# Optimization experiments

Measured on AMD Instinct MI355X. Metric: run time of the kernel, lower is better.

## Reference

```python
import jax, jax.numpy as jnp
import numpy as np


def setup_inputs() -> dict:
    key = jax.random.key(0)
    k1, k2 = jax.random.split(key)
    n, d, ic, oc, r = 128, 256, 16, 16, 10
    x = jax.random.normal(k1, (n, d, ic, r), dtype=jnp.float32)
    weights = jax.random.normal(k2, (d, ic, oc, r), dtype=jnp.float32)
    return {"x": x, "weights": weights}


def reference(x, weights):
    # x: [n, d, ic, r]; weights: [d, ic, oc, r]
    # log_softmax over in_channels (dim=1 of weights)
    log_weights = jax.nn.log_softmax(weights, axis=1)  # [d, ic, oc, r]
    # broadcast add: x[n,d,ic,1,r] + lw[d,ic,oc,r] -> [n,d,ic,oc,r]
    z = x[:, :, :, None, :] + log_weights[None]
    # logsumexp over ic -> [n, d, oc, r]
    return jax.nn.logsumexp(z, axis=2)
```

## Files before the change

kernel.cpp:

```cpp
#include <hip/hip_runtime.h>
#include <hip/hip_bf16.h>


typedef __attribute__((ext_vector_type(8))) short bf16x8;
typedef __attribute__((ext_vector_type(4))) float f32x4;

__device__ __forceinline__ unsigned short f2bf(float v) {
    unsigned u = __float_as_uint(v);
    u += 0x7FFF + ((u >> 16) & 1);
    return (unsigned short)(u >> 16);
}

__global__ __launch_bounds__(512, 2) void fused_mfma_kernel(const float* __restrict__ x,
                                                            const float* __restrict__ w,
                                                            float* __restrict__ out) {
    __shared__ __align__(16) unsigned short es[128 * 328];
    __shared__ __align__(16) unsigned short ws_[10 * 640];
    __shared__ float lcs[160];

    const int tid = threadIdx.x;
    const int d   = blockIdx.x;

    {
        const int n_l = tid >> 2;
        const int seg = tid & 3;
        const float* xg = x + (n_l * 256 + d) * 160 + seg * 40;
        float4 xv[10];
#pragma unroll
        for (int k = 0; k < 10; ++k) xv[k] = *reinterpret_cast<const float4*>(xg + 4 * k);
        const float* wgp = w + d * 2560 + tid * 5;
        float wv[5];
#pragma unroll
        for (int k = 0; k < 5; ++k) wv[k] = wgp[k];

        const float* xf = reinterpret_cast<const float*>(xv);
#pragma unroll
        for (int k = 0; k < 40; ++k) {
            const int icr = seg * 40 + k;
            const int ic  = icr / 10;
            const int r   = icr - ic * 10;
            es[n_l * 328 + r * 32 + ic] = f2bf(__expf(xf[k]));
        }
#pragma unroll
        for (int k = 0; k < 5; ++k) {
            const int off = tid * 5 + k;
            const int ic  = off / 160;
            const int rem = off - ic * 160;
            const int oc  = rem / 10;
            const int r   = rem - oc * 10;
            ws_[r * 640 + oc * 40 + ic] = f2bf(__expf(wv[k]));
        }
        const uint4 z = make_uint4(0u, 0u, 0u, 0u);
        for (int c = tid; c < 1280; c += 512) {
            const int n = c / 10, r = c - (c / 10) * 10;
            uint4* p = reinterpret_cast<uint4*>(&es[n * 328 + r * 32 + 16]);
            p[0] = z; p[1] = z;
        }
        if (tid < 160) {
            const int r = tid >> 4, oc = tid & 15;
            uint4* p = reinterpret_cast<uint4*>(&ws_[r * 640 + oc * 40 + 16]);
            p[0] = z; p[1] = z;
        }
    }
    __syncthreads();

    if (tid < 160) {
        const int oc = tid / 10, r = tid - (tid / 10) * 10;
        const unsigned short* p = &ws_[r * 640 + oc * 40];
        float s = 0.f;
#pragma unroll
        for (int ic = 0; ic < 16; ++ic)
            s += __uint_as_float(((unsigned)p[ic]) << 16);
        lcs[oc * 10 + r] = __logf(s);
    }

    const int mt = tid >> 6;
    const int l  = tid & 63;
    const int lm = l & 15;
    const int kg = l >> 4;

    const int abase = (mt * 16 + lm) * 328 + kg * 8;
    const int bbase = lm * 40 + kg * 8;

    f32x4 acc[10];
    const f32x4 zero = {0.f, 0.f, 0.f, 0.f};
#pragma unroll
    for (int r = 0; r < 10; ++r) {
        bf16x8 a = *reinterpret_cast<const bf16x8*>(&es[abase + r * 32]);
        bf16x8 b = *reinterpret_cast<const bf16x8*>(&ws_[r * 640 + bbase]);
        acc[r] = __builtin_amdgcn_mfma_f32_16x16x32_bf16(a, b, zero, 0, 0, 0);
    }
    __syncthreads();

    float lc[10];
#pragma unroll
    for (int r = 0; r < 10; ++r) lc[r] = lcs[lm * 10 + r];

#pragma unroll
    for (int j = 0; j < 4; ++j) {
        const int n = mt * 16 + kg * 4 + j;
        float* og = out + (n * 256 + d) * 160 + lm * 10;
#pragma unroll
        for (int h = 0; h < 5; ++h) {
            float2 o;
            o.x = __logf(acc[2 * h][j])     - lc[2 * h];
            o.y = __logf(acc[2 * h + 1][j]) - lc[2 * h + 1];
            *reinterpret_cast<float2*>(og + 2 * h) = o;
        }
    }
}

extern "C" void kernel_launch(void* const* d_in, const int* in_sizes, int n_in,
                              void* d_out, int out_size, void* d_ws, size_t ws_size,
                              hipStream_t stream) {
    const float* x = (const float*)d_in[0];
    const float* w = (const float*)d_in[1];
    float* out = (float*)d_out;

    fused_mfma_kernel<<<256, 512, 0, stream>>>(x, w, out);
}
```

Baseline: 17.99 us.

## Split weight preprocessing into prep kernel and regrid main kernel to smaller blocks

```diff
diff --git a/kernel.cpp b/kernel.cpp
--- a/kernel.cpp
+++ b/kernel.cpp
@@ -5,101 +5,127 @@
 typedef __attribute__((ext_vector_type(8))) short bf16x8;
 typedef __attribute__((ext_vector_type(4))) float f32x4;
 
+#define LCS_OFF 1310720
+
 __device__ __forceinline__ unsigned short f2bf(float v) {
     unsigned u = __float_as_uint(v);
     u += 0x7FFF + ((u >> 16) & 1);
     return (unsigned short)(u >> 16);
 }
 
-__global__ __launch_bounds__(512, 2) void fused_mfma_kernel(const float* __restrict__ x,
-                                                            const float* __restrict__ w,
-                                                            float* __restrict__ out) {
-    __shared__ __align__(16) unsigned short es[128 * 328];
-    __shared__ __align__(16) unsigned short ws_[10 * 640];
-    __shared__ float lcs[160];
+__global__ __launch_bounds__(256) void prep_kernel(const float* __restrict__ w,
+                                                   void* __restrict__ ws) {
+    __shared__ float lexp[2560];
+    const int d   = blockIdx.x;
+    const int tid = threadIdx.x;
+    const int ic  = tid >> 4, oc = tid & 15;
 
-    const int tid = threadIdx.x;
-    const int d   = blockIdx.x;
+    const float* wp = w + d * 2560 + ic * 160 + oc * 10;
+#pragma unroll
+    for (int k = 0; k < 5; ++k) {
+        float2 v = *reinterpret_cast<const float2*>(wp + 2 * k);
+        lexp[tid * 10 + 2 * k]     = __expf(v.x);
+        lexp[tid * 10 + 2 * k + 1] = __expf(v.y);
+    }
+    __syncthreads();
+
+    if (tid < 160) {
+        const int o2 = tid / 10, rr = tid - (tid / 10) * 10;
+        float s = 0.f;
+#pragma unroll
+        for (int i2 = 0; i2 < 16; ++i2) s += lexp[(i2 * 16 + o2) * 10 + rr];
+        float* lcs = reinterpret_cast<float*>(reinterpret_cast<char*>(ws) + LCS_OFF);
+        lcs[d * 160 + tid] = __logf(s);
+    }
+
+    unsigned* wf = reinterpret_cast<unsigned*>(ws);
+    const int idx    = tid & 127;
+    const int lane32 = idx >> 2;
+    const int wsel   = idx & 3;
+    const int kg     = lane32 >> 4;
+    const int oc2    = lane32 & 15;
+    const int s0     = kg * 8 + wsel * 2;
+#pragma unroll
+    for (int rr2 = 0; rr2 < 5; ++rr2) {
+        const int r = rr2 * 2 + (tid >> 7);
+        const unsigned lo = f2bf(lexp[(s0 * 16 + oc2) * 10 + r]);
+        const unsigned hi = f2bf(lexp[((s0 + 1) * 16 + oc2) * 10 + r]);
+        wf[(d * 10 + r) * 128 + idx] = lo | (hi << 16);
+    }
+}
+
+__global__ __launch_bounds__(128, 3) void main_kernel(const float* __restrict__ x,
+                                                      const void* __restrict__ ws,
+                                                      float* __restrict__ out) {
+    __shared__ __align__(16) unsigned short es[32 * 328];
+
+    const int tid  = threadIdx.x;
+    const int dg   = blockIdx.x & 127;
+    const int nc   = blockIdx.x >> 7;
+    const int wid  = tid >> 6;
+    const int lane = tid & 63;
+    const int lm   = lane & 15;
+    const int kg   = lane >> 4;
+    const int d_g  = dg * 2 + wid;
+    const int n_b  = nc * 16;
+
+    bf16x8 bfr[10];
+    const unsigned* wf = reinterpret_cast<const unsigned*>(ws);
+#pragma unroll
+    for (int r = 0; r < 10; ++r) {
+        if (lane < 32) {
+            bfr[r] = *reinterpret_cast<const bf16x8*>(&wf[(d_g * 10 + r) * 128 + lane * 4]);
+        } else {
+            bfr[r] = bf16x8{0, 0, 0, 0, 0, 0, 0, 0};
+        }
+    }
+    float lc[10];
+    {
+        const float* lcs = reinterpret_cast<const float*>(
+            reinterpret_cast<const char*>(ws) + LCS_OFF) + d_g * 160 + lm * 10;
+#pragma unroll
+        for (int k = 0; k < 5; ++k) {
+            float2 v = *reinterpret_cast<const float2*>(lcs + 2 * k);
+            lc[2 * k] = v.x; lc[2 * k + 1] = v.y;
+        }
+    }
 
     {
-        const int n_l = tid >> 2;
-        const int seg = tid & 3;
-        const float* xg = x + (n_l * 256 + d) * 160 + seg * 40;
+        const int n_l = tid >> 3;
+        const int sub = tid & 7;
+        const int d_l = sub >> 2;
+        const int seg = sub & 3;
+        const float* xg = x + ((n_b + n_l) * 256 + dg * 2 + d_l) * 160 + seg * 40;
         float4 xv[10];
 #pragma unroll
         for (int k = 0; k < 10; ++k) xv[k] = *reinterpret_cast<const float4*>(xg + 4 * k);
-        const float* wgp = w + d * 2560 + tid * 5;
-        float wv[5];
+        const float* xf = reinterpret_cast<const float*>(xv);
+        const int row = d_l * 16 + n_l;
 #pragma unroll
-        for (int k = 0; k < 5; ++k) wv[k] = wgp[k];
-
-        const float* xf = reinterpret_cast<const float*>(xv);
-#pragma unroll
-        for (int k = 0; k < 40; ++k) {
-            const int icr = seg * 40 + k;
-            const int ic  = icr / 10;
-            const int r   = icr - ic * 10;
-            es[n_l * 328 + r * 32 + ic] = f2bf(__expf(xf[k]));
-        }
-#pragma unroll
-        for (int k = 0; k < 5; ++k) {
-            const int off = tid * 5 + k;
-            const int ic  = off / 160;
-            const int rem = off - ic * 160;
-            const int oc  = rem / 10;
-            const int r   = rem - oc * 10;
-            ws_[r * 640 + oc * 40 + ic] = f2bf(__expf(wv[k]));
-        }
-        const uint4 z = make_uint4(0u, 0u, 0u, 0u);
-        for (int c = tid; c < 1280; c += 512) {
-            const int n = c / 10, r = c - (c / 10) * 10;
-            uint4* p = reinterpret_cast<uint4*>(&es[n * 328 + r * 32 + 16]);
-            p[0] = z; p[1] = z;
-        }
-        if (tid < 160) {
-            const int r = tid >> 4, oc = tid & 15;
-            uint4* p = reinterpret_cast<uint4*>(&ws_[r * 640 + oc * 40 + 16]);
-            p[0] = z; p[1] = z;
+        for (int r = 0; r < 10; ++r) {
+            const unsigned lo = (unsigned)f2bf(__expf(xf[r]))      | ((unsigned)f2bf(__expf(xf[10 + r])) << 16);
+            const unsigned hi = (unsigned)f2bf(__expf(xf[20 + r])) | ((unsigned)f2bf(__expf(xf[30 + r])) << 16);
+            unsigned* dst = reinterpret_cast<unsigned*>(&es[row * 328 + r * 32 + seg * 4]);
+            *reinterpret_cast<uint2*>(dst) = make_uint2(lo, hi);
+            unsigned* pad = reinterpret_cast<unsigned*>(&es[row * 328 + r * 32 + 16 + seg * 4]);
+            *reinterpret_cast<uint2*>(pad) = make_uint2(0u, 0u);
         }
     }
     __syncthreads();
 
-    if (tid < 160) {
-        const int oc = tid / 10, r = tid - (tid / 10) * 10;
-        const unsigned short* p = &ws_[r * 640 + oc * 40];
-        float s = 0.f;
-#pragma unroll
-        for (int ic = 0; ic < 16; ++ic)
-            s += __uint_as_float(((unsigned)p[ic]) << 16);
-        lcs[oc * 10 + r] = __logf(s);
-    }
-
-    const int mt = tid >> 6;
-    const int l  = tid & 63;
-    const int lm = l & 15;
-    const int kg = l >> 4;
-
-    const int abase = (mt * 16 + lm) * 328 + kg * 8;
-    const int bbase = lm * 40 + kg * 8;
-
+    const int abase = (wid * 16 + lm) * 328 + kg * 8;
     f32x4 acc[10];
     const f32x4 zero = {0.f, 0.f, 0.f, 0.f};
 #pragma unroll
     for (int r = 0; r < 10; ++r) {
         bf16x8 a = *reinterpret_cast<const bf16x8*>(&es[abase + r * 32]);
-        bf16x8 b = *reinterpret_cast<const bf16x8*>(&ws_[r * 640 + bbase]);
-        acc[r] = __builtin_amdgcn_mfma_f32_16x16x32_bf16(a, b, zero, 0, 0, 0);
+        acc[r] = __builtin_amdgcn_mfma_f32_16x16x32_bf16(a, bfr[r], zero, 0, 0, 0);
     }
-    __syncthreads();
-
-    float lc[10];
-#pragma unroll
-    for (int r = 0; r < 10; ++r) lc[r] = lcs[lm * 10 + r];
 
 #pragma unroll
     for (int j = 0; j < 4; ++j) {
-        const int n = mt * 16 + kg * 4 + j;
-        float* og = out + (n * 256 + d) * 160 + lm * 10;
+        const int n = n_b + kg * 4 + j;
+        float* og = out + (n * 256 + d_g) * 160 + lm * 10;
 #pragma unroll
         for (int h = 0; h < 5; ++h) {
             float2 o;
@@ -117,5 +143,6 @@
     const float* w = (const float*)d_in[1];
     float* out = (float*)d_out;
 
-    fused_mfma_kernel<<<256, 512, 0, stream>>>(x, w, out);
+    prep_kernel<<<256, 256, 0, stream>>>(w, d_ws);
+    main_kernel<<<1024, 128, 0, stream>>>(x, d_ws, out);
 }
```

Measured after the change: 20.02 us. 1.11x slower.
